# Optimization experiments

Hardware: AMD Instinct MI355X
Metric: run time of the kernel (lower is better)

The kernel has to match this reference:

```python
import jax, jax.numpy as jnp
import numpy as np
from jax import lax

B = 16        # point clouds per batch
NPC = 4096    # points per cloud (N = B*NPC = 65536)
M_PC = 1024   # centroids per cloud after FPS (ratio=0.25)
K = 64        # max_num_neighbors (hardcoded in module)
R = 0.2       # radius
F_IN = 64     # input feature dim


def _fps(p, m):
    """Farthest point sampling on p:[n,3] -> m int32 indices (deterministic, start at 0)."""
    n = p.shape[0]
    def step(carry, _):
        d, last = carry
        nd = jnp.minimum(d, jnp.sum((p - p[last]) ** 2, axis=-1))
        return (nd, jnp.argmax(nd).astype(jnp.int32)), last
    (_, _), idxs = lax.scan(step, (jnp.full((n,), jnp.inf, p.dtype), jnp.int32(0)), None, length=m)
    return idxs


def setup_inputs() -> dict:
    key = jax.random.key(0)
    k0, k1, k2, k3 = jax.random.split(key, 4)
    N = B * NPC
    x = jax.random.normal(k0, (N, F_IN), jnp.float32)
    pos = jax.random.uniform(k1, (N, 3), jnp.float32)  # unit cube -> r=0.2 balls are well populated
    batch = jnp.repeat(jnp.arange(B, dtype=jnp.int32), NPC)
    W1 = jax.random.normal(k2, (F_IN + 3, 64), jnp.float32) * 0.1
    b1 = jnp.zeros((64,), jnp.float32)
    W2 = jax.random.normal(k3, (64, 128), jnp.float32) * 0.1
    b2 = jnp.zeros((128,), jnp.float32)
    return {"x": x, "pos": pos, "batch": batch, "W1": W1, "b1": b1, "W2": W2, "b2": b2}


def reference(x, pos, batch, W1, b1, W2, b2):
    pos_b = pos.reshape(B, NPC, 3)
    x_b = x.reshape(B, NPC, F_IN)

    # 1. FPS sampling per cloud -> centroid indices [B, M_PC]
    idx = jax.vmap(lambda p: _fps(p, M_PC))(pos_b)
    pos_c = jnp.take_along_axis(pos_b, idx[:, :, None], axis=1)  # [B,M,3]

    # 2. radius neighbor search: K nearest within R per centroid (same cloud only)
    d2 = jnp.sum((pos_c[:, :, None, :] - pos_b[:, None, :, :]) ** 2, axis=-1)  # [B,M,NPC]
    neg, nidx = lax.top_k(-d2, K)           # K smallest distances
    valid = (-neg) <= R * R                 # [B,M,K] inside-ball mask

    # 3. PointNetConv: gather, per-edge MLP on [x_j, pos_j - pos_i], max-aggregate
    x_j = jax.vmap(lambda xb, ib: xb[ib])(x_b, nidx)    # [B,M,K,F_IN]
    p_j = jax.vmap(lambda pb, ib: pb[ib])(pos_b, nidx)  # [B,M,K,3]
    rel = p_j - pos_c[:, :, None, :]
    feat = jnp.concatenate([x_j, rel], axis=-1)          # [B,M,K,F_IN+3]
    h = jax.nn.relu(feat @ W1 + b1)
    h = h @ W2 + b2                                      # plain last layer (PyG MLP default)
    h = jnp.where(valid[..., None], h, -jnp.inf)
    out = jnp.max(h, axis=2)                             # [B,M,128]
    out = jnp.where(jnp.any(valid, axis=2)[..., None], out, 0.0)

    out = out.reshape(B * M_PC, -1)
    pos_out = pos_c.reshape(B * M_PC, 3)
    batch_out = jnp.repeat(jnp.arange(B, dtype=batch.dtype), M_PC)
    return out, pos_out, batch_out
```

## Files before the change

kernel.cpp:

```cpp
#include <hip/hip_runtime.h>

#define NB   16
#define NPC  4096
#define MPC  1024
#define KNB  64
#define FIN  64
#define CAP  448

typedef unsigned short u16;
typedef unsigned int   u32;
typedef unsigned long long u64;
typedef __attribute__((ext_vector_type(8))) short short8;
typedef __attribute__((ext_vector_type(4))) float f32x4;

__device__ __forceinline__ u16 f2bf(float f) {
  u32 u = __float_as_uint(f);
  u = u + 0x7fffu + ((u >> 16) & 1u);
  return (u16)(u >> 16);
}
__device__ __forceinline__ float bf2f(u16 b) {
  return __uint_as_float(((u32)b) << 16);
}

__device__ __forceinline__ u32 wave_max_u32(u32 x) {
  u32 t;
  t = (u32)__builtin_amdgcn_update_dpp((int)x, (int)x, 0x111, 0xf, 0xf, false); x = x > t ? x : t;
  t = (u32)__builtin_amdgcn_update_dpp((int)x, (int)x, 0x112, 0xf, 0xf, false); x = x > t ? x : t;
  t = (u32)__builtin_amdgcn_update_dpp((int)x, (int)x, 0x114, 0xf, 0xf, false); x = x > t ? x : t;
  t = (u32)__builtin_amdgcn_update_dpp((int)x, (int)x, 0x118, 0xf, 0xf, false); x = x > t ? x : t;
  t = (u32)__builtin_amdgcn_update_dpp((int)x, (int)x, 0x142, 0xa, 0xf, false); x = x > t ? x : t;
  t = (u32)__builtin_amdgcn_update_dpp((int)x, (int)x, 0x143, 0xc, 0xf, false); x = x > t ? x : t;
  return x;
}
__device__ __forceinline__ u32 wave_min_u32(u32 x) {
  u32 t;
  t = (u32)__builtin_amdgcn_update_dpp((int)x, (int)x, 0x111, 0xf, 0xf, false); x = x < t ? x : t;
  t = (u32)__builtin_amdgcn_update_dpp((int)x, (int)x, 0x112, 0xf, 0xf, false); x = x < t ? x : t;
  t = (u32)__builtin_amdgcn_update_dpp((int)x, (int)x, 0x114, 0xf, 0xf, false); x = x < t ? x : t;
  t = (u32)__builtin_amdgcn_update_dpp((int)x, (int)x, 0x118, 0xf, 0xf, false); x = x < t ? x : t;
  t = (u32)__builtin_amdgcn_update_dpp((int)x, (int)x, 0x142, 0xa, 0xf, false); x = x < t ? x : t;
  t = (u32)__builtin_amdgcn_update_dpp((int)x, (int)x, 0x143, 0xc, 0xf, false); x = x < t ? x : t;
  return x;
}

__global__ __launch_bounds__(512)
void fps_kernel(const float* __restrict__ pos, int* __restrict__ idx_out,
                float* __restrict__ pos_out, float* __restrict__ batch_out) {
  const int b = blockIdx.x;
  const int t = threadIdx.x;
  const float* P = pos + (size_t)b * NPC * 3;
  __shared__ float sx[NPC], sy[NPC], sz[NPC];
  __shared__ u64 swave[2][8];
  for (int i = t; i < NPC; i += 512) {
    sx[i] = P[3*i+0]; sy[i] = P[3*i+1]; sz[i] = P[3*i+2];
  }
  for (int i = t; i < MPC; i += 512) batch_out[b*MPC + i] = (float)b;
  __syncthreads();
  float px[8], py[8], pz[8], mind[8];
#pragma unroll
  for (int r = 0; r < 8; ++r) {
    int i = t + (r << 9);
    px[r] = sx[i]; py[r] = sy[i]; pz[r] = sz[i];
    mind[r] = __builtin_inff();
  }
  int last = 0;
  if (t == 0) {
    idx_out[b*MPC] = 0;
    pos_out[(size_t)b*MPC*3 + 0] = sx[0];
    pos_out[(size_t)b*MPC*3 + 1] = sy[0];
    pos_out[(size_t)b*MPC*3 + 2] = sz[0];
  }
  for (int m = 1; m < MPC; ++m) {
    float cx = sx[last], cy = sy[last], cz = sz[last];
    u32 vmax = 0;
#pragma unroll
    for (int r = 0; r < 8; ++r) {
      float dx = __fsub_rn(px[r], cx);
      float dy = __fsub_rn(py[r], cy);
      float dz = __fsub_rn(pz[r], cz);
      float d2 = __fadd_rn(__fadd_rn(__fmul_rn(dx,dx), __fmul_rn(dy,dy)), __fmul_rn(dz,dz));
      mind[r] = fminf(mind[r], d2);
      u32 bits = __float_as_uint(mind[r]);
      vmax = bits > vmax ? bits : vmax;
    }
    vmax = wave_max_u32(vmax);
    u32 V = (u32)__builtin_amdgcn_readlane((int)vmax, 63);
    u32 cand = 0xffffffffu;
#pragma unroll
    for (int r = 7; r >= 0; --r)
      cand = (__float_as_uint(mind[r]) == V) ? (u32)(t + (r << 9)) : cand;
    cand = wave_min_u32(cand);
    if ((t & 63) == 63) swave[m & 1][t >> 6] = ((u64)V << 32) | (u32)(~cand);
    __syncthreads();
    u64 w = swave[m & 1][0];
#pragma unroll
    for (int q = 1; q < 8; ++q) {
      u64 o = swave[m & 1][q];
      w = o > w ? o : w;
    }
    last = (int)(~(u32)w);
    if (t == 0) {
      idx_out[b*MPC + m] = last;
      size_t po = ((size_t)b*MPC + m)*3;
      pos_out[po+0] = sx[last]; pos_out[po+1] = sy[last]; pos_out[po+2] = sz[last];
    }
  }
}

__global__ __launch_bounds__(256)
void y_kernel(const float* __restrict__ x, const float* __restrict__ w1,
              u16* __restrict__ y) {
  __shared__ float xs[64][68];
  __shared__ float ws[64][68];
  const int t = threadIdx.x;
  const size_t row0 = (size_t)blockIdx.x * 64;
#pragma unroll
  for (int k = 0; k < 4; ++k) {
    int l = t + 256*k;
    int r = l >> 4, c4 = l & 15;
    *(float4*)&xs[r][c4*4] = *(const float4*)&x[(row0 + r)*64 + c4*4];
    *(float4*)&ws[r][c4*4] = *(const float4*)&w1[r*64 + c4*4];
  }
  __syncthreads();
  const int r = t >> 2, c0 = (t & 3) << 4;
  float acc[16];
#pragma unroll
  for (int i = 0; i < 16; ++i) acc[i] = 0.f;
  for (int k = 0; k < 64; ++k) {
    float a = xs[r][k];
#pragma unroll
    for (int j = 0; j < 4; ++j) {
      float4 wv = *(const float4*)&ws[k][c0 + 4*j];
      acc[4*j+0] += a * wv.x; acc[4*j+1] += a * wv.y;
      acc[4*j+2] += a * wv.z; acc[4*j+3] += a * wv.w;
    }
  }
  u32 u[8];
#pragma unroll
  for (int i = 0; i < 8; ++i)
    u[i] = (u32)f2bf(acc[2*i]) | ((u32)f2bf(acc[2*i+1]) << 16);
  u16* dst = y + ((row0 + r)*64 + c0);
  ((uint4*)dst)[0] = make_uint4(u[0],u[1],u[2],u[3]);
  ((uint4*)dst)[1] = make_uint4(u[4],u[5],u[6],u[7]);
}

__global__ __launch_bounds__(256)
void w2t_kernel(const float* __restrict__ w2, u16* __restrict__ w2t) {
  int t = blockIdx.x*256 + threadIdx.x;
  if (t < 64*128) {
    int k = t >> 7, c = t & 127;
    w2t[c*64 + k] = f2bf(w2[t]);
  }
}

__global__ __launch_bounds__(256)
void nbr_kernel(const float* __restrict__ pos, const int* __restrict__ idx,
                int* __restrict__ nbr, int* __restrict__ nvalid) {
  const int bid = blockIdx.x;
  const int sw = (bid & 7) * 512 + (bid >> 3);
  const int cloud = sw >> 8;
  const int mbase = (sw & 255) << 2;
  __shared__ float sx[NPC], sy[NPC], sz[NPC];
  __shared__ u64 cand[4][CAP];
  const float* P = pos + (size_t)cloud * NPC * 3;
  const int t = threadIdx.x;
  for (int i = t; i < NPC; i += 256) { sx[i]=P[3*i]; sy[i]=P[3*i+1]; sz[i]=P[3*i+2]; }
  __syncthreads();
  const int wv = t >> 6, lane = t & 63;
  const int m = mbase + wv;
  const int g = cloud * MPC + m;
  const int ci = idx[g];
  const float cx = sx[ci], cy = sy[ci], cz = sz[ci];
  const float R2 = 0.04000000059604644775f;
  const u64 ltmask = (lane == 0) ? 0ull : (~0ull >> (64 - lane));
  int base = 0;
  for (int i = 0; i < NPC/64; ++i) {
    int j = (i << 6) + lane;
    float dx = __fsub_rn(cx, sx[j]);
    float dy = __fsub_rn(cy, sy[j]);
    float dz = __fsub_rn(cz, sz[j]);
    float d2 = __fadd_rn(__fadd_rn(__fmul_rn(dx,dx), __fmul_rn(dy,dy)), __fmul_rn(dz,dz));
    bool in = d2 <= R2;
    u64 mk = __ballot(in);
    if (in) {
      int slot = base + (int)__popcll(mk & ltmask);
      if (slot < CAP)
        cand[wv][slot] = ((u64)__float_as_uint(d2) << 32) | (u32)j;
    }
    base += (int)__popcll(mk);
  }
  int cnt = base < CAP ? base : CAP;
  u64 mykey[7];
  int myrank[7];
#pragma unroll
  for (int u = 0; u < 7; ++u) {
    int s = lane + (u << 6);
    mykey[u] = (s < cnt) ? cand[wv][s] : ~0ull;
    myrank[u] = 0;
  }
  for (int jj = 0; jj < cnt; ++jj) {
    u64 kj = cand[wv][jj];
#pragma unroll
    for (int u = 0; u < 7; ++u) myrank[u] += (kj < mykey[u]) ? 1 : 0;
  }
#pragma unroll
  for (int u = 0; u < 7; ++u) {
    int s = lane + (u << 6);
    if (s < cnt && myrank[u] < KNB)
      nbr[(size_t)g*KNB + myrank[u]] = cloud*NPC + (int)(mykey[u] & 0xffffffffull);
  }
  if (lane == 0) nvalid[g] = cnt < KNB ? cnt : KNB;
}

__global__ __launch_bounds__(256)
void conv_kernel(const float* __restrict__ pos, const int* __restrict__ idx,
                 const int* __restrict__ nbr, const int* __restrict__ nvalid,
                 const u16* __restrict__ y, const u16* __restrict__ w2t,
                 const float* __restrict__ w1, const float* __restrict__ b1,
                 const float* __restrict__ b2, float* __restrict__ out) {
  const int bid = blockIdx.x;
  const int g = (bid & 7) * 2048 + (bid >> 3);
  const int cloud = g >> 10;
  __shared__ u16 YH[64][72];
  __shared__ u16 WT[128][72];
  __shared__ float rel[64][3];
  __shared__ int nbs[64];
  __shared__ float w1p[192];
  __shared__ float b1s[64];
  const int t = threadIdx.x;
  const int nv = nvalid[g];
  if (t < 64) nbs[t] = (t < nv) ? nbr[(size_t)g*KNB + t] : -1;
  if (t < 192) w1p[t] = w1[64*64 + t];
  else         b1s[t - 192] = b1[t - 192];
  __syncthreads();
  if (t < 64) {
    int ci = cloud*NPC + idx[g];
    float cxx = pos[3*ci], cyy = pos[3*ci+1], czz = pos[3*ci+2];
    int j = nbs[t];
    float r0 = 0.f, r1 = 0.f, r2 = 0.f;
    if (t < nv && j >= 0) {
      r0 = pos[3*j]   - cxx;
      r1 = pos[3*j+1] - cyy;
      r2 = pos[3*j+2] - czz;
    }
    rel[t][0] = r0; rel[t][1] = r1; rel[t][2] = r2;
  }
  {
    int row = t >> 2, part = t & 3;
    int j = nbs[row];
    uint4 v0 = make_uint4(0,0,0,0), v1 = make_uint4(0,0,0,0);
    if (row < nv && j >= 0) {
      const uint4* src = (const uint4*)(y + (size_t)j*64);
      v0 = src[part*2]; v1 = src[part*2 + 1];
    }
    *(uint4*)&YH[row][part*16]     = v0;
    *(uint4*)&YH[row][part*16 + 8] = v1;
  }
#pragma unroll
  for (int k = 0; k < 4; ++k) {
    int l = t + 256*k;
    int row = l >> 3, part = l & 7;
    *(uint4*)&WT[row][part*8] = ((const uint4*)w2t)[l];
  }
  __syncthreads();
  {
    int s = t >> 2, c0 = (t & 3) << 4;
    float rx = rel[s][0], ry = rel[s][1], rz = rel[s][2];
#pragma unroll
    for (int c = 0; c < 16; ++c) {
      int cc = c0 + c;
      float v = bf2f(YH[s][cc]) + rx*w1p[cc] + ry*w1p[64+cc] + rz*w1p[128+cc] + b1s[cc];
      v = fmaxf(v, 0.f);
      YH[s][cc] = f2bf(v);
    }
  }
  __syncthreads();
  const int wv = t >> 6, lane = t & 63;
  const int arow = lane & 15, agrp = lane >> 4;
  const int col0 = wv << 5;
  f32x4 acc[4][2];
#pragma unroll
  for (int mt = 0; mt < 4; ++mt)
#pragma unroll
    for (int nt = 0; nt < 2; ++nt) {
      f32x4 z = {0.f, 0.f, 0.f, 0.f};
      acc[mt][nt] = z;
    }
#pragma unroll
  for (int kk = 0; kk < 2; ++kk) {
    short8 a[4], bm[2];
#pragma unroll
    for (int mt = 0; mt < 4; ++mt)
      a[mt] = *(const short8*)&YH[mt*16 + arow][kk*32 + agrp*8];
#pragma unroll
    for (int nt = 0; nt < 2; ++nt)
      bm[nt] = *(const short8*)&WT[col0 + nt*16 + arow][kk*32 + agrp*8];
#pragma unroll
    for (int mt = 0; mt < 4; ++mt)
#pragma unroll
      for (int nt = 0; nt < 2; ++nt)
        acc[mt][nt] = __builtin_amdgcn_mfma_f32_16x16x32_bf16(a[mt], bm[nt], acc[mt][nt], 0, 0, 0);
  }
  float p0 = -__builtin_inff(), p1 = -__builtin_inff();
#pragma unroll
  for (int mt = 0; mt < 4; ++mt) {
#pragma unroll
    for (int r = 0; r < 4; ++r) {
      int slot = mt*16 + agrp*4 + r;
      if (slot < nv) {
        p0 = fmaxf(p0, acc[mt][0][r]);
        p1 = fmaxf(p1, acc[mt][1][r]);
      }
    }
  }
  p0 = fmaxf(p0, __shfl_xor(p0, 16, 64));
  p0 = fmaxf(p0, __shfl_xor(p0, 32, 64));
  p1 = fmaxf(p1, __shfl_xor(p1, 16, 64));
  p1 = fmaxf(p1, __shfl_xor(p1, 32, 64));
  if (lane < 16) {
    int c = col0 + lane;
    out[(size_t)g*128 + c]      = (nv > 0) ? p0 + b2[c]      : 0.f;
    out[(size_t)g*128 + c + 16] = (nv > 0) ? p1 + b2[c + 16] : 0.f;
  }
}

extern "C" void kernel_launch(void* const* d_in, const int* in_sizes, int n_in,
                              void* d_out, int out_size, void* d_ws, size_t ws_size,
                              hipStream_t stream) {
  const float* x   = (const float*)d_in[0];
  const float* pos = (const float*)d_in[1];
  const float* W1  = (const float*)d_in[3];
  const float* b1  = (const float*)d_in[4];
  const float* W2  = (const float*)d_in[5];
  const float* b2  = (const float*)d_in[6];

  float* out       = (float*)d_out;
  float* pos_out   = out + (size_t)NB*MPC*128;
  float* batch_out = pos_out + (size_t)NB*MPC*3;

  char* ws = (char*)d_ws;
  int* idx    = (int*)(ws);
  int* nvalid = (int*)(ws + 65536);
  int* nbr    = (int*)(ws + 131072);
  u16* w2t    = (u16*)(ws + 131072 + 4194304);
  u16* y      = (u16*)(ws + 131072 + 4194304 + 16384);

  fps_kernel <<<NB,    512,  0, stream>>>(pos, idx, pos_out, batch_out);
  y_kernel   <<<1024,  256,  0, stream>>>(x, W1, y);
  w2t_kernel <<<32,    256,  0, stream>>>(W2, w2t);
  nbr_kernel <<<4096,  256,  0, stream>>>(pos, idx, nbr, nvalid);
  conv_kernel<<<16384, 256,  0, stream>>>(pos, idx, nbr, nvalid, y, w2t, W1, b1, b2, out);
}
```

Baseline: 899.1 us.

## Spatially bucket FPS points and skip buckets whose bounding box cannot lower minimum distance

The farthest-point-sampling kernel now sorts each cloud's points into 64 spatial cells, assigns each wave two buckets of 256 spatially coherent points, and records a bounding box per bucket. On each iteration a bucket whose box lower bound on distance to the new centroid exceeds its current max of min-distances is skipped, and its cached best key is reused. This cuts distance updates and reductions in the serial 1023-step loop. In exchange it adds setup cost, extra shared memory and divergent per-wave control flow, and it relies on a 0.999 slack factor to keep tie-breaking exact.

```diff
diff --git a/kernel.cpp b/kernel.cpp
--- a/kernel.cpp
+++ b/kernel.cpp
@@ -6,6 +6,7 @@
 #define KNB  64
 #define FIN  64
 #define CAP  448
+#define NBKT 16
 
 typedef unsigned short u16;
 typedef unsigned int   u32;
@@ -21,6 +22,20 @@
 __device__ __forceinline__ float bf2f(u16 b) {
   return __uint_as_float(((u32)b) << 16);
 }
+
+#define DPP64_MAX(best, ctrl, rmask) do { \
+  u32 _lo = (u32)(best), _hi = (u32)((best) >> 32); \
+  u32 _olo = (u32)__builtin_amdgcn_update_dpp((int)_lo, (int)_lo, (ctrl), (rmask), 0xf, false); \
+  u32 _ohi = (u32)__builtin_amdgcn_update_dpp((int)_hi, (int)_hi, (ctrl), (rmask), 0xf, false); \
+  u64 _o = ((u64)_ohi << 32) | _olo; \
+  (best) = _o > (best) ? _o : (best); \
+} while (0)
+
+#define DPP64_MAX_ALL(k) do { \
+  DPP64_MAX(k, 0x111, 0xf); DPP64_MAX(k, 0x112, 0xf); \
+  DPP64_MAX(k, 0x114, 0xf); DPP64_MAX(k, 0x118, 0xf); \
+  DPP64_MAX(k, 0x142, 0xa); DPP64_MAX(k, 0x143, 0xc); \
+} while (0)
 
 __device__ __forceinline__ u32 wave_max_u32(u32 x) {
   u32 t;
@@ -43,25 +58,83 @@
   return x;
 }
 
+__device__ __forceinline__ int cell_of(float x, float y, float z) {
+  int ix = (int)(x * 4.f); ix = ix < 0 ? 0 : (ix > 3 ? 3 : ix);
+  int iy = (int)(y * 4.f); iy = iy < 0 ? 0 : (iy > 3 ? 3 : iy);
+  int iz = (int)(z * 4.f); iz = iz < 0 ? 0 : (iz > 3 ? 3 : iz);
+  return (ix & 1) | ((iy & 1) << 1) | ((iz & 1) << 2)
+       | ((ix >> 1) << 3) | ((iy >> 1) << 4) | ((iz >> 1) << 5);
+}
+
 __global__ __launch_bounds__(512)
 void fps_kernel(const float* __restrict__ pos, int* __restrict__ idx_out,
                 float* __restrict__ pos_out, float* __restrict__ batch_out) {
   const int b = blockIdx.x;
   const int t = threadIdx.x;
+  const int w = t >> 6, lane = t & 63;
   const float* P = pos + (size_t)b * NPC * 3;
   __shared__ float sx[NPC], sy[NPC], sz[NPC];
-  __shared__ u64 swave[2][8];
+  __shared__ int   slist[NPC];
+  __shared__ int   hist[64], cellbase[64];
+  __shared__ float bbox[NBKT][6];
+  __shared__ u64   bst[2][NBKT];
+  __shared__ u64   wmax[2][8];
   for (int i = t; i < NPC; i += 512) {
     sx[i] = P[3*i+0]; sy[i] = P[3*i+1]; sz[i] = P[3*i+2];
   }
   for (int i = t; i < MPC; i += 512) batch_out[b*MPC + i] = (float)b;
+  if (t < 64) hist[t] = 0;
+  __syncthreads();
+  for (int p = t; p < NPC; p += 512)
+    atomicAdd(&hist[cell_of(sx[p], sy[p], sz[p])], 1);
+  __syncthreads();
+  if (t == 0) {
+    int run = 0;
+    for (int c = 0; c < 64; ++c) { cellbase[c] = run; run += hist[c]; }
+  }
+  __syncthreads();
+  if (t < 64) hist[t] = 0;
+  __syncthreads();
+  for (int p = t; p < NPC; p += 512) {
+    int c = cell_of(sx[p], sy[p], sz[p]);
+    int r = cellbase[c] + atomicAdd(&hist[c], 1);
+    slist[r] = p;
+  }
   __syncthreads();
   float px[8], py[8], pz[8], mind[8];
-#pragma unroll
-  for (int r = 0; r < 8; ++r) {
-    int i = t + (r << 9);
-    px[r] = sx[i]; py[r] = sy[i]; pz[r] = sz[i];
-    mind[r] = __builtin_inff();
+  int oi[8];
+#pragma unroll
+  for (int q = 0; q < 2; ++q)
+#pragma unroll
+    for (int j = 0; j < 4; ++j) {
+      int r = (q << 2) | j;
+      int s = ((w << 1) | q) * 256 + (j << 6) + lane;
+      int o = slist[s];
+      oi[r] = o; px[r] = sx[o]; py[r] = sy[o]; pz[r] = sz[o];
+      mind[r] = __builtin_inff();
+    }
+#pragma unroll
+  for (int q = 0; q < 2; ++q) {
+    int r0 = q << 2;
+    float mn0 = fminf(fminf(px[r0], px[r0+1]), fminf(px[r0+2], px[r0+3]));
+    float mx0 = fmaxf(fmaxf(px[r0], px[r0+1]), fmaxf(px[r0+2], px[r0+3]));
+    float mn1 = fminf(fminf(py[r0], py[r0+1]), fminf(py[r0+2], py[r0+3]));
+    float mx1 = fmaxf(fmaxf(py[r0], py[r0+1]), fmaxf(py[r0+2], py[r0+3]));
+    float mn2 = fminf(fminf(pz[r0], pz[r0+1]), fminf(pz[r0+2], pz[r0+3]));
+    float mx2 = fmaxf(fmaxf(pz[r0], pz[r0+1]), fmaxf(pz[r0+2], pz[r0+3]));
+    u32 a0 = wave_min_u32(__float_as_uint(mn0));
+    u32 a1 = wave_max_u32(__float_as_uint(mx0));
+    u32 a2 = wave_min_u32(__float_as_uint(mn1));
+    u32 a3 = wave_max_u32(__float_as_uint(mx1));
+    u32 a4 = wave_min_u32(__float_as_uint(mn2));
+    u32 a5 = wave_max_u32(__float_as_uint(mx2));
+    if (lane == 63) {
+      int bkt = (w << 1) | q;
+      bbox[bkt][0] = __uint_as_float(a0); bbox[bkt][1] = __uint_as_float(a1);
+      bbox[bkt][2] = __uint_as_float(a2); bbox[bkt][3] = __uint_as_float(a3);
+      bbox[bkt][4] = __uint_as_float(a4); bbox[bkt][5] = __uint_as_float(a5);
+      bst[0][bkt] = ((u64)0x7f800000u << 32);
+    }
   }
   int last = 0;
   if (t == 0) {
@@ -70,35 +143,53 @@
     pos_out[(size_t)b*MPC*3 + 1] = sy[0];
     pos_out[(size_t)b*MPC*3 + 2] = sz[0];
   }
+  __syncthreads();
   for (int m = 1; m < MPC; ++m) {
-    float cx = sx[last], cy = sy[last], cz = sz[last];
-    u32 vmax = 0;
-#pragma unroll
-    for (int r = 0; r < 8; ++r) {
-      float dx = __fsub_rn(px[r], cx);
-      float dy = __fsub_rn(py[r], cy);
-      float dz = __fsub_rn(pz[r], cz);
-      float d2 = __fadd_rn(__fadd_rn(__fmul_rn(dx,dx), __fmul_rn(dy,dy)), __fmul_rn(dz,dz));
-      mind[r] = fminf(mind[r], d2);
-      u32 bits = __float_as_uint(mind[r]);
-      vmax = bits > vmax ? bits : vmax;
-    }
-    vmax = wave_max_u32(vmax);
-    u32 V = (u32)__builtin_amdgcn_readlane((int)vmax, 63);
-    u32 cand = 0xffffffffu;
-#pragma unroll
-    for (int r = 7; r >= 0; --r)
-      cand = (__float_as_uint(mind[r]) == V) ? (u32)(t + (r << 9)) : cand;
-    cand = wave_min_u32(cand);
-    if ((t & 63) == 63) swave[m & 1][t >> 6] = ((u64)V << 32) | (u32)(~cand);
+    const int pr = m & 1, pv = pr ^ 1;
+    const float cx = sx[last], cy = sy[last], cz = sz[last];
+    u64 mywave = 0;
+#pragma unroll
+    for (int q = 0; q < 2; ++q) {
+      const int bkt = (w << 1) | q;
+      u64 old = bst[pv][bkt];
+      float bmax = __uint_as_float((u32)(old >> 32));
+      float t0 = fmaxf(fmaxf(bbox[bkt][0] - cx, cx - bbox[bkt][1]), 0.f);
+      float t1 = fmaxf(fmaxf(bbox[bkt][2] - cy, cy - bbox[bkt][3]), 0.f);
+      float t2 = fmaxf(fmaxf(bbox[bkt][4] - cz, cz - bbox[bkt][5]), 0.f);
+      float bound = (t0*t0 + t1*t1) + t2*t2;
+      u64 nk;
+      if (bound * 0.999f >= bmax) {
+        nk = old;
+      } else {
+        u64 kk = 0;
+#pragma unroll
+        for (int j = 0; j < 4; ++j) {
+          int r = (q << 2) | j;
+          float dx = __fsub_rn(px[r], cx);
+          float dy = __fsub_rn(py[r], cy);
+          float dz = __fsub_rn(pz[r], cz);
+          float d2 = __fadd_rn(__fadd_rn(__fmul_rn(dx,dx), __fmul_rn(dy,dy)), __fmul_rn(dz,dz));
+          mind[r] = fminf(mind[r], d2);
+          u64 key = ((u64)__float_as_uint(mind[r]) << 32) | (u32)(~(u32)oi[r]);
+          kk = key > kk ? key : kk;
+        }
+        DPP64_MAX_ALL(kk);
+        nk = kk;
+      }
+      if (lane == 63) {
+        bst[pr][bkt] = nk;
+        mywave = mywave > nk ? mywave : nk;
+      }
+    }
+    if (lane == 63) wmax[pr][w] = mywave;
     __syncthreads();
-    u64 w = swave[m & 1][0];
-#pragma unroll
-    for (int q = 1; q < 8; ++q) {
-      u64 o = swave[m & 1][q];
-      w = o > w ? o : w;
-    }
-    last = (int)(~(u32)w);
+    u64 W = wmax[pr][0];
+#pragma unroll
+    for (int qq = 1; qq < 8; ++qq) {
+      u64 o = wmax[pr][qq];
+      W = o > W ? o : W;
+    }
+    last = (int)(~(u32)W);
     if (t == 0) {
       idx_out[b*MPC + m] = last;
       size_t po = ((size_t)b*MPC + m)*3;
```

Measured after the change: 1.087 ms. 20.9% more time.

## Fuse FPS, input projection and W2 transpose into one launch

Applied to the files above, without the earlier changes.

Merges the FPS kernel, the x@W1 projection kernel and the W2 transpose kernel into a single launch. The 16 FPS blocks run alongside the 1024 projection blocks, so the long serial FPS loop overlaps with independent work instead of leaving most CUs idle. The FPS loop also now stores its indices in shared memory and writes idx/pos_out in one parallel pass at the end, rather than having thread 0 issue global stores every iteration. The shared-memory union sizes every block for the FPS footprint, which may lower occupancy for the projection blocks.

```diff
diff --git a/kernel.cpp b/kernel.cpp
--- a/kernel.cpp
+++ b/kernel.cpp
@@ -43,113 +43,111 @@
   return x;
 }
 
+struct FpsLDS {
+  float sx[NPC], sy[NPC], sz[NPC];
+  u64 swave[2][8];
+  int sidx[MPC];
+};
+struct YLDS { float xs[64][68]; float ws[64][68]; };
+union FusedLDS { FpsLDS f; YLDS g; };
+
 __global__ __launch_bounds__(512)
-void fps_kernel(const float* __restrict__ pos, int* __restrict__ idx_out,
-                float* __restrict__ pos_out, float* __restrict__ batch_out) {
-  const int b = blockIdx.x;
+void fused_kernel(const float* __restrict__ pos, const float* __restrict__ x,
+                  const float* __restrict__ w1, const float* __restrict__ w2,
+                  int* __restrict__ idx_out, float* __restrict__ pos_out,
+                  float* __restrict__ batch_out, u16* __restrict__ y,
+                  u16* __restrict__ w2t) {
+  __shared__ FusedLDS L;
+  const int bid = blockIdx.x;
   const int t = threadIdx.x;
-  const float* P = pos + (size_t)b * NPC * 3;
-  __shared__ float sx[NPC], sy[NPC], sz[NPC];
-  __shared__ u64 swave[2][8];
-  for (int i = t; i < NPC; i += 512) {
-    sx[i] = P[3*i+0]; sy[i] = P[3*i+1]; sz[i] = P[3*i+2];
-  }
-  for (int i = t; i < MPC; i += 512) batch_out[b*MPC + i] = (float)b;
-  __syncthreads();
-  float px[8], py[8], pz[8], mind[8];
-#pragma unroll
-  for (int r = 0; r < 8; ++r) {
-    int i = t + (r << 9);
-    px[r] = sx[i]; py[r] = sy[i]; pz[r] = sz[i];
-    mind[r] = __builtin_inff();
-  }
-  int last = 0;
-  if (t == 0) {
-    idx_out[b*MPC] = 0;
-    pos_out[(size_t)b*MPC*3 + 0] = sx[0];
-    pos_out[(size_t)b*MPC*3 + 1] = sy[0];
-    pos_out[(size_t)b*MPC*3 + 2] = sz[0];
-  }
-  for (int m = 1; m < MPC; ++m) {
-    float cx = sx[last], cy = sy[last], cz = sz[last];
-    u32 vmax = 0;
+  if (bid < NB) {
+    const int b = bid;
+    const float* P = pos + (size_t)b * NPC * 3;
+    for (int i = t; i < NPC; i += 512) {
+      L.f.sx[i] = P[3*i+0]; L.f.sy[i] = P[3*i+1]; L.f.sz[i] = P[3*i+2];
+    }
+    for (int i = t; i < MPC; i += 512) batch_out[b*MPC + i] = (float)b;
+    if (t == 0) L.f.sidx[0] = 0;
+    __syncthreads();
+    float px[8], py[8], pz[8], mind[8];
 #pragma unroll
     for (int r = 0; r < 8; ++r) {
-      float dx = __fsub_rn(px[r], cx);
-      float dy = __fsub_rn(py[r], cy);
-      float dz = __fsub_rn(pz[r], cz);
-      float d2 = __fadd_rn(__fadd_rn(__fmul_rn(dx,dx), __fmul_rn(dy,dy)), __fmul_rn(dz,dz));
-      mind[r] = fminf(mind[r], d2);
-      u32 bits = __float_as_uint(mind[r]);
-      vmax = bits > vmax ? bits : vmax;
-    }
-    vmax = wave_max_u32(vmax);
-    u32 V = (u32)__builtin_amdgcn_readlane((int)vmax, 63);
-    u32 cand = 0xffffffffu;
-#pragma unroll
-    for (int r = 7; r >= 0; --r)
-      cand = (__float_as_uint(mind[r]) == V) ? (u32)(t + (r << 9)) : cand;
-    cand = wave_min_u32(cand);
-    if ((t & 63) == 63) swave[m & 1][t >> 6] = ((u64)V << 32) | (u32)(~cand);
+      int i = t + (r << 9);
+      px[r] = L.f.sx[i]; py[r] = L.f.sy[i]; pz[r] = L.f.sz[i];
+      mind[r] = __builtin_inff();
+    }
+    int last = 0;
+    for (int m = 1; m < MPC; ++m) {
+      float cx = L.f.sx[last], cy = L.f.sy[last], cz = L.f.sz[last];
+      u32 vmax = 0;
+#pragma unroll
+      for (int r = 0; r < 8; ++r) {
+        float dx = __fsub_rn(px[r], cx);
+        float dy = __fsub_rn(py[r], cy);
+        float dz = __fsub_rn(pz[r], cz);
+        float d2 = __fadd_rn(__fadd_rn(__fmul_rn(dx,dx), __fmul_rn(dy,dy)), __fmul_rn(dz,dz));
+        mind[r] = fminf(mind[r], d2);
+        u32 bits = __float_as_uint(mind[r]);
+        vmax = bits > vmax ? bits : vmax;
+      }
+      vmax = wave_max_u32(vmax);
+      u32 V = (u32)__builtin_amdgcn_readlane((int)vmax, 63);
+      u32 cand = 0xffffffffu;
+#pragma unroll
+      for (int r = 7; r >= 0; --r)
+        cand = (__float_as_uint(mind[r]) == V) ? (u32)(t + (r << 9)) : cand;
+      cand = wave_min_u32(cand);
+      if ((t & 63) == 63) L.f.swave[m & 1][t >> 6] = ((u64)V << 32) | (u32)(~cand);
+      __syncthreads();
+      u64 w = L.f.swave[m & 1][0];
+#pragma unroll
+      for (int q = 1; q < 8; ++q) {
+        u64 o = L.f.swave[m & 1][q];
+        w = o > w ? o : w;
+      }
+      last = (int)(~(u32)w);
+      if (t == 0) L.f.sidx[m] = last;
+    }
     __syncthreads();
-    u64 w = swave[m & 1][0];
-#pragma unroll
-    for (int q = 1; q < 8; ++q) {
-      u64 o = swave[m & 1][q];
-      w = o > w ? o : w;
-    }
-    last = (int)(~(u32)w);
-    if (t == 0) {
-      idx_out[b*MPC + m] = last;
-      size_t po = ((size_t)b*MPC + m)*3;
-      pos_out[po+0] = sx[last]; pos_out[po+1] = sy[last]; pos_out[po+2] = sz[last];
-    }
-  }
-}
-
-__global__ __launch_bounds__(256)
-void y_kernel(const float* __restrict__ x, const float* __restrict__ w1,
-              u16* __restrict__ y) {
-  __shared__ float xs[64][68];
-  __shared__ float ws[64][68];
-  const int t = threadIdx.x;
-  const size_t row0 = (size_t)blockIdx.x * 64;
-#pragma unroll
-  for (int k = 0; k < 4; ++k) {
-    int l = t + 256*k;
-    int r = l >> 4, c4 = l & 15;
-    *(float4*)&xs[r][c4*4] = *(const float4*)&x[(row0 + r)*64 + c4*4];
-    *(float4*)&ws[r][c4*4] = *(const float4*)&w1[r*64 + c4*4];
-  }
-  __syncthreads();
-  const int r = t >> 2, c0 = (t & 3) << 4;
-  float acc[16];
-#pragma unroll
-  for (int i = 0; i < 16; ++i) acc[i] = 0.f;
-  for (int k = 0; k < 64; ++k) {
-    float a = xs[r][k];
-#pragma unroll
-    for (int j = 0; j < 4; ++j) {
-      float4 wv = *(const float4*)&ws[k][c0 + 4*j];
-      acc[4*j+0] += a * wv.x; acc[4*j+1] += a * wv.y;
-      acc[4*j+2] += a * wv.z; acc[4*j+3] += a * wv.w;
-    }
-  }
-  u32 u[8];
-#pragma unroll
-  for (int i = 0; i < 8; ++i)
-    u[i] = (u32)f2bf(acc[2*i]) | ((u32)f2bf(acc[2*i+1]) << 16);
-  u16* dst = y + ((row0 + r)*64 + c0);
-  ((uint4*)dst)[0] = make_uint4(u[0],u[1],u[2],u[3]);
-  ((uint4*)dst)[1] = make_uint4(u[4],u[5],u[6],u[7]);
-}
-
-__global__ __launch_bounds__(256)
-void w2t_kernel(const float* __restrict__ w2, u16* __restrict__ w2t) {
-  int t = blockIdx.x*256 + threadIdx.x;
-  if (t < 64*128) {
-    int k = t >> 7, c = t & 127;
-    w2t[c*64 + k] = f2bf(w2[t]);
+    for (int i = t; i < MPC; i += 512) {
+      int ii = L.f.sidx[i];
+      idx_out[b*MPC + i] = ii;
+      size_t po = ((size_t)b*MPC + i)*3;
+      pos_out[po+0] = L.f.sx[ii];
+      pos_out[po+1] = L.f.sy[ii];
+      pos_out[po+2] = L.f.sz[ii];
+    }
+  } else if (bid < NB + 1024) {
+    const size_t row0 = (size_t)(bid - NB) * 64;
+#pragma unroll
+    for (int k = 0; k < 2; ++k) {
+      int l4 = t + 512*k;
+      int r = l4 >> 4, c4 = l4 & 15;
+      *(float4*)&L.g.xs[r][c4*4] = *(const float4*)&x[(row0 + r)*64 + c4*4];
+      *(float4*)&L.g.ws[r][c4*4] = *(const float4*)&w1[r*64 + c4*4];
+    }
+    __syncthreads();
+    const int r = t >> 3, c0 = (t & 7) << 3;
+    float acc[8];
+#pragma unroll
+    for (int i = 0; i < 8; ++i) acc[i] = 0.f;
+    for (int k = 0; k < 64; ++k) {
+      float a = L.g.xs[r][k];
+      float4 w0 = *(const float4*)&L.g.ws[k][c0];
+      float4 w1v = *(const float4*)&L.g.ws[k][c0 + 4];
+      acc[0] += a * w0.x; acc[1] += a * w0.y; acc[2] += a * w0.z; acc[3] += a * w0.w;
+      acc[4] += a * w1v.x; acc[5] += a * w1v.y; acc[6] += a * w1v.z; acc[7] += a * w1v.w;
+    }
+    u32 u[4];
+#pragma unroll
+    for (int i = 0; i < 4; ++i)
+      u[i] = (u32)f2bf(acc[2*i]) | ((u32)f2bf(acc[2*i+1]) << 16);
+    *(uint4*)(y + ((row0 + r)*64 + c0)) = make_uint4(u[0], u[1], u[2], u[3]);
+  } else {
+    for (int i = t; i < 64*128; i += 512) {
+      int k = i >> 7, c = i & 127;
+      w2t[c*64 + k] = f2bf(w2[i]);
+    }
   }
 }
 
@@ -345,9 +343,8 @@
   u16* w2t    = (u16*)(ws + 131072 + 4194304);
   u16* y      = (u16*)(ws + 131072 + 4194304 + 16384);
 
-  fps_kernel <<<NB,    512,  0, stream>>>(pos, idx, pos_out, batch_out);
-  y_kernel   <<<1024,  256,  0, stream>>>(x, W1, y);
-  w2t_kernel <<<32,    256,  0, stream>>>(W2, w2t);
+  fused_kernel<<<NB + 1024 + 1, 512, 0, stream>>>(pos, x, W1, W2, idx, pos_out,
+                                                  batch_out, y, w2t);
   nbr_kernel <<<4096,  256,  0, stream>>>(pos, idx, nbr, nvalid);
   conv_kernel<<<16384, 256,  0, stream>>>(pos, idx, nbr, nvalid, y, w2t, W1, b1, b2, out);
 }
```

After: 912.7 us. About the same (+1.5%).
